# Kernel tuning notes

Hardware: AMD Instinct MI355X
Metric: run time of the kernel (lower is better)

## Reference

```python
import jax, jax.numpy as jnp
import numpy as np

N = 50000      # nodes
E = 800000     # edges (avg degree 16)
D = 128        # embed_dim
H = 8          # nhead
HD = D // H    # head dim = 16


def setup_inputs() -> dict:
    key = jax.random.key(0)
    ks = jax.random.split(key, 6)
    s = 1.0 / np.sqrt(D)  # ~xavier scale for square matrices
    return {
        "feats": jax.random.normal(ks[0], (N, D), jnp.float32),
        "edge_index": jax.random.randint(ks[1], (E, 2), 0, N, dtype=jnp.int64),
        "Wq": jax.random.normal(ks[2], (D, D), jnp.float32) * s,
        "bq": jnp.zeros((D,), jnp.float32),
        "Wk": jax.random.normal(ks[3], (D, D), jnp.float32) * s,
        "bk": jnp.zeros((D,), jnp.float32),
        "Wv": jax.random.normal(ks[4], (D, D), jnp.float32) * s,
        "bv": jnp.zeros((D,), jnp.float32),
        "Wo": jax.random.normal(ks[5], (D, D), jnp.float32) * s,
        "bo": jnp.zeros((D,), jnp.float32),
    }


def reference(feats, edge_index, Wq, bq, Wk, bk, Wv, bv, Wo, bo):
    # Projections (nn.Linear: x @ W.T + b), split into heads: [N, H, HD]
    q = (feats @ Wq.T + bq).reshape(N, H, HD)
    k = (feats @ Wk.T + bk).reshape(N, H, HD)
    v = (feats @ Wv.T + bv).reshape(N, H, HD)

    r = edge_index[:, 0]  # source nodes
    c = edge_index[:, 1]  # destination nodes (softmax / aggregation groups)

    # Per-edge, per-head dot-product scores: [E, H]
    scores = jnp.einsum('ehd,ehd->eh', q[c], k[r]) / np.sqrt(HD)

    # Custom scatter-softmax: src_max clamped to min 0; extra exp(-src_max) in denom
    smax = jnp.maximum(jax.ops.segment_max(scores, c, num_segments=N), 0.0)  # [N, H]
    ex = jnp.exp(scores - smax[c])                                           # [E, H]
    denom = jax.ops.segment_sum(ex, c, num_segments=N)                       # [N, H]
    attn = ex / (denom + jnp.exp(-smax))[c]                                  # [E, H]

    # Weighted V per edge, scatter-mean to destination nodes
    out_e = attn[:, :, None] * v[r]                      # [E, H, HD]
    agg = jax.ops.segment_sum(out_e, c, num_segments=N)  # [N, H, HD]
    cnt = jax.ops.segment_sum(jnp.ones((E,), jnp.float32), c, num_segments=N)
    agg = agg / jnp.maximum(cnt, 1.0)[:, None, None]

    return agg.reshape(N, D) @ Wo.T + bo
```

## Files before the change

kernel.cpp:

```cpp
#include <hip/hip_runtime.h>
#include <hip/hip_bf16.h>

#define N_NODES 50000
#define N_EDGES 800000
#define DIM 128
#define NHEAD 8
#define HDIM 16
#define ELL_PAD 64

#define Q_OFF      0ull
#define KV_OFF     25600000ull
#define AGG_OFF    51200000ull
#define ELL_OFF    64000000ull
#define WBF_OFF    76800000ull
#define BIAS_OFF   76931072ull
#define CNT_OFF    76933376ull

typedef __attribute__((ext_vector_type(8))) short short8;
typedef __attribute__((ext_vector_type(4))) float floatx4;

__device__ inline float bflo2f(unsigned u) { return __uint_as_float(u << 16); }
__device__ inline float bfhi2f(unsigned u) { return __uint_as_float(u & 0xffff0000u); }
__device__ inline unsigned short f2bf(float f) {
    unsigned u = __float_as_uint(f);
    return (unsigned short)((u + 0x7fffu + ((u >> 16) & 1u)) >> 16);
}

__device__ inline void detect_flags(const void* feats, const void* edge,
                                    int& isbf, int& is32) {
    const unsigned short* f = (const unsigned short*)feats;
    const unsigned int* eg = (const unsigned int*)edge;
    int lane = threadIdx.x & 63;
    unsigned e = (f[lane] >> 7) & 0xFF;
    int junk = (e >= 0x90 || (e > 0 && e <= 0x60)) ? 1 : 0;
    unsigned long long jm = __ballot(junk);
    int nz = (lane < 32 && eg[2 * lane + 1] != 0) ? 1 : 0;
    unsigned long long nm = __ballot(nz);
    isbf = (jm == 0ull) ? 1 : 0;
    is32 = (nm != 0ull) ? 1 : 0;
}

__device__ inline void load_edge(const int* edge, int is32, int e, int& r, int& c) {
    if (is32) { r = edge[2 * e]; c = edge[2 * e + 1]; }
    else {
        const long long* p = (const long long*)edge;
        r = (int)p[2 * e]; c = (int)p[2 * e + 1];
    }
    if ((unsigned)r >= N_NODES) r = 0;
    if ((unsigned)c >= N_NODES) c = 0;
}

__global__ __launch_bounds__(256) void prep_wb(const void* feats, const int* edge,
                                               const void* wq, const void* wk,
                                               const void* wv, const void* wo,
                                               const void* bq, const void* bk,
                                               const void* bv, const void* bo,
                                               unsigned short* wbf, float* bias, int* cnt) {
    int isbf, is32; detect_flags(feats, edge, isbf, is32);
    int b = blockIdx.x, t = threadIdx.x;
    if (b < 196) {
        int i = b * 256 + t;
        if (i < N_NODES) cnt[i] = 0;
    }
    if (b == 256) {
        for (int j = t; j < 512; j += 256) {
            int m2 = j >> 7, c2 = j & 127;
            const void* bb = (m2 == 0) ? bq : (m2 == 1) ? bk : (m2 == 2) ? bv : bo;
            bias[j] = isbf ? __bfloat162float(((const __hip_bfloat16*)bb)[c2])
                           : ((const float*)bb)[c2];
        }
        return;
    }
    if (isbf) return;
    int idx = b * 256 + t;
    int m = idx >> 14, rem = idx & 16383;
    const void* w = (m == 0) ? wq : (m == 1) ? wk : (m == 2) ? wv : wo;
    wbf[idx] = f2bf(((const float*)w)[rem]);
}

__global__ __launch_bounds__(256) void ell_build(const void* feats, const int* edge,
                                                 int* cnt, int* ell) {
    int isbf, is32; detect_flags(feats, edge, isbf, is32);
    int e0 = (blockIdx.x * 256 + threadIdx.x) * 2;
    #pragma unroll
    for (int j = 0; j < 2; ++j) {
        int e = e0 + j;
        if (e >= N_EDGES) return;
        int r, c; load_edge(edge, is32, e, r, c);
        int slot = atomicAdd(cnt + c, 1);
        if (slot < ELL_PAD) ell[c * ELL_PAD + slot] = r;
    }
}

__global__ __launch_bounds__(256) void qkv_mfma(const void* feats_raw, const int* edge,
                                                const void* wq_raw, const void* wk_raw,
                                                const void* wv_raw, const unsigned short* wbf,
                                                const float* bias,
                                                float* q, unsigned int* kvpack) {
    int isbf, is32; detect_flags(feats_raw, edge, isbf, is32);
    const unsigned short* W[3];
    W[0] = isbf ? (const unsigned short*)wq_raw : wbf;
    W[1] = isbf ? (const unsigned short*)wk_raw : wbf + 16384;
    W[2] = isbf ? (const unsigned short*)wv_raw : wbf + 32768;

    int wave = threadIdx.x >> 6, lane = threadIdx.x & 63;
    int rbase = blockIdx.x * 64 + wave * 16;
    int mrow = lane & 15, quad = lane >> 4;
    int arow = rbase + mrow; if (arow >= N_NODES) arow = N_NODES - 1;

    short8 a[4];
    if (isbf) {
        const unsigned short* ap = (const unsigned short*)feats_raw + (size_t)arow * DIM + quad * 8;
        #pragma unroll
        for (int kt = 0; kt < 4; ++kt) a[kt] = *(const short8*)(ap + kt * 32);
    } else {
        const float* af = (const float*)feats_raw + (size_t)arow * DIM + quad * 8;
        #pragma unroll
        for (int kt = 0; kt < 4; ++kt) {
            float4 f0 = *(const float4*)(af + kt * 32);
            float4 f1 = *(const float4*)(af + kt * 32 + 4);
            a[kt][0] = (short)f2bf(f0.x); a[kt][1] = (short)f2bf(f0.y);
            a[kt][2] = (short)f2bf(f0.z); a[kt][3] = (short)f2bf(f0.w);
            a[kt][4] = (short)f2bf(f1.x); a[kt][5] = (short)f2bf(f1.y);
            a[kt][6] = (short)f2bf(f1.z); a[kt][7] = (short)f2bf(f1.w);
        }
    }

    for (int m = 0; m < 3; ++m) {
        const unsigned short* wm = W[m];
        for (int nt = 0; nt < 8; ++nt) {
            const unsigned short* wp = wm + (size_t)(nt * 16 + mrow) * DIM + quad * 8;
            float b = bias[m * 128 + nt * 16 + mrow];
            floatx4 acc = {b, b, b, b};
            #pragma unroll
            for (int kt = 0; kt < 4; ++kt) {
                short8 bf = *(const short8*)(wp + kt * 32);
                acc = __builtin_amdgcn_mfma_f32_16x16x32_bf16(a[kt], bf, acc, 0, 0, 0);
            }
            if (m == 0) {
                #pragma unroll
                for (int r4 = 0; r4 < 4; ++r4) {
                    int row = rbase + quad * 4 + r4;
                    if (row < N_NODES) q[(size_t)row * DIM + nt * 16 + mrow] = acc[r4];
                }
            } else {
                int sel = (m == 2) ? 8 : 0;
                #pragma unroll
                for (int r4 = 0; r4 < 4; ++r4) {
                    float other = __shfl_xor(acc[r4], 1);
                    int row = rbase + quad * 4 + r4;
                    if (((lane & 1) == 0) && row < N_NODES) {
                        unsigned packed = (unsigned)f2bf(acc[r4]) | ((unsigned)f2bf(other) << 16);
                        kvpack[(size_t)row * 128 + nt * 16 + sel + (mrow >> 1)] = packed;
                    }
                }
            }
        }
    }
}

__global__ __launch_bounds__(256) void node_agg(const int* __restrict__ cnt,
                                                const int* __restrict__ ell,
                                                const float* __restrict__ q,
                                                const uint4* __restrict__ kvpack,
                                                uint4* __restrict__ agg_bf) {
    int node = (blockIdx.x * 256 + threadIdx.x) >> 6;
    int lane = threadIdx.x & 63;
    if (node >= N_NODES) return;
    int e = lane >> 3, h = lane & 7;

    float qv[16];
    const float4* qp = (const float4*)(q + (size_t)node * DIM + h * HDIM);
    #pragma unroll
    for (int i = 0; i < 4; ++i) {
        float4 tq = qp[i];
        qv[4 * i] = tq.x; qv[4 * i + 1] = tq.y; qv[4 * i + 2] = tq.z; qv[4 * i + 3] = tq.w;
    }

    int degt = cnt[node];
    int deg = degt < ELL_PAD ? degt : ELL_PAD;
    float l = 0.f;
    float acc[16];
    #pragma unroll
    for (int i = 0; i < 16; ++i) acc[i] = 0.f;

    const int* erow = ell + node * ELL_PAD;
    for (int i0 = 0; i0 < deg; i0 += 16) {
        int i1 = i0 + e, i2 = i0 + 8 + e;
        bool ok1 = i1 < deg, ok2 = i2 < deg;
        int r1 = ok1 ? erow[i1] : 0;
        int r2 = ok2 ? erow[i2] : 0;
        const uint4* kp1 = kvpack + (size_t)r1 * 32 + h * 4;
        const uint4* kp2 = kvpack + (size_t)r2 * 32 + h * 4;
        uint4 ka1 = kp1[0], kb1 = kp1[1], va1 = kp1[2], vb1 = kp1[3];
        uint4 ka2 = kp2[0], kb2 = kp2[1], va2 = kp2[2], vb2 = kp2[3];

        float s1 = 0.f;
        s1 += bflo2f(ka1.x) * qv[0]  + bfhi2f(ka1.x) * qv[1];
        s1 += bflo2f(ka1.y) * qv[2]  + bfhi2f(ka1.y) * qv[3];
        s1 += bflo2f(ka1.z) * qv[4]  + bfhi2f(ka1.z) * qv[5];
        s1 += bflo2f(ka1.w) * qv[6]  + bfhi2f(ka1.w) * qv[7];
        s1 += bflo2f(kb1.x) * qv[8]  + bfhi2f(kb1.x) * qv[9];
        s1 += bflo2f(kb1.y) * qv[10] + bfhi2f(kb1.y) * qv[11];
        s1 += bflo2f(kb1.z) * qv[12] + bfhi2f(kb1.z) * qv[13];
        s1 += bflo2f(kb1.w) * qv[14] + bfhi2f(kb1.w) * qv[15];
        float p1 = ok1 ? __expf(s1 * 0.25f) : 0.f;
        l += p1;
        acc[0]  += p1 * bflo2f(va1.x); acc[1]  += p1 * bfhi2f(va1.x);
        acc[2]  += p1 * bflo2f(va1.y); acc[3]  += p1 * bfhi2f(va1.y);
        acc[4]  += p1 * bflo2f(va1.z); acc[5]  += p1 * bfhi2f(va1.z);
        acc[6]  += p1 * bflo2f(va1.w); acc[7]  += p1 * bfhi2f(va1.w);
        acc[8]  += p1 * bflo2f(vb1.x); acc[9]  += p1 * bfhi2f(vb1.x);
        acc[10] += p1 * bflo2f(vb1.y); acc[11] += p1 * bfhi2f(vb1.y);
        acc[12] += p1 * bflo2f(vb1.z); acc[13] += p1 * bfhi2f(vb1.z);
        acc[14] += p1 * bflo2f(vb1.w); acc[15] += p1 * bfhi2f(vb1.w);

        float s2 = 0.f;
        s2 += bflo2f(ka2.x) * qv[0]  + bfhi2f(ka2.x) * qv[1];
        s2 += bflo2f(ka2.y) * qv[2]  + bfhi2f(ka2.y) * qv[3];
        s2 += bflo2f(ka2.z) * qv[4]  + bfhi2f(ka2.z) * qv[5];
        s2 += bflo2f(ka2.w) * qv[6]  + bfhi2f(ka2.w) * qv[7];
        s2 += bflo2f(kb2.x) * qv[8]  + bfhi2f(kb2.x) * qv[9];
        s2 += bflo2f(kb2.y) * qv[10] + bfhi2f(kb2.y) * qv[11];
        s2 += bflo2f(kb2.z) * qv[12] + bfhi2f(kb2.z) * qv[13];
        s2 += bflo2f(kb2.w) * qv[14] + bfhi2f(kb2.w) * qv[15];
        float p2 = ok2 ? __expf(s2 * 0.25f) : 0.f;
        l += p2;
        acc[0]  += p2 * bflo2f(va2.x); acc[1]  += p2 * bfhi2f(va2.x);
        acc[2]  += p2 * bflo2f(va2.y); acc[3]  += p2 * bfhi2f(va2.y);
        acc[4]  += p2 * bflo2f(va2.z); acc[5]  += p2 * bfhi2f(va2.z);
        acc[6]  += p2 * bflo2f(va2.w); acc[7]  += p2 * bfhi2f(va2.w);
        acc[8]  += p2 * bflo2f(vb2.x); acc[9]  += p2 * bfhi2f(vb2.x);
        acc[10] += p2 * bflo2f(vb2.y); acc[11] += p2 * bfhi2f(vb2.y);
        acc[12] += p2 * bflo2f(vb2.z); acc[13] += p2 * bfhi2f(vb2.z);
        acc[14] += p2 * bflo2f(vb2.w); acc[15] += p2 * bfhi2f(vb2.w);
    }

    #pragma unroll
    for (int m = 8; m < 64; m <<= 1) {
        l += __shfl_xor(l, m);
        #pragma unroll
        for (int i = 0; i < 16; ++i) acc[i] += __shfl_xor(acc[i], m);
    }

    float inv = 1.0f / ((1.0f + l) * (float)(degt > 0 ? degt : 1));
    if (e == 0) {
        unsigned o[8];
        #pragma unroll
        for (int i = 0; i < 8; ++i)
            o[i] = (unsigned)f2bf(acc[2 * i] * inv) | ((unsigned)f2bf(acc[2 * i + 1] * inv) << 16);
        uint4* op = agg_bf + (size_t)node * 16 + h * 2;
        op[0] = make_uint4(o[0], o[1], o[2], o[3]);
        op[1] = make_uint4(o[4], o[5], o[6], o[7]);
    }
}

__global__ __launch_bounds__(256) void out_mfma(const unsigned short* agg_bf,
                                                const void* feats, const int* edge,
                                                const void* wo_raw, const unsigned short* wbf,
                                                const float* bias, void* out) {
    int isbf, is32; detect_flags(feats, edge, isbf, is32);
    const unsigned short* W = isbf ? (const unsigned short*)wo_raw : wbf + 49152;
    int wave = threadIdx.x >> 6, lane = threadIdx.x & 63;
    int rbase = blockIdx.x * 64 + wave * 16;
    int mrow = lane & 15, quad = lane >> 4;
    int arow = rbase + mrow; if (arow >= N_NODES) arow = N_NODES - 1;

    short8 a[4];
    const unsigned short* ap = agg_bf + (size_t)arow * DIM + quad * 8;
    #pragma unroll
    for (int kt = 0; kt < 4; ++kt) a[kt] = *(const short8*)(ap + kt * 32);

    for (int nt = 0; nt < 8; ++nt) {
        const unsigned short* wp = W + (size_t)(nt * 16 + mrow) * DIM + quad * 8;
        float b = bias[3 * 128 + nt * 16 + mrow];
        floatx4 acc = {b, b, b, b};
        #pragma unroll
        for (int kt = 0; kt < 4; ++kt) {
            short8 bf = *(const short8*)(wp + kt * 32);
            acc = __builtin_amdgcn_mfma_f32_16x16x32_bf16(a[kt], bf, acc, 0, 0, 0);
        }
        if (isbf) {
            #pragma unroll
            for (int r4 = 0; r4 < 4; ++r4) {
                float other = __shfl_xor(acc[r4], 1);
                int row = rbase + quad * 4 + r4;
                if (((lane & 1) == 0) && row < N_NODES) {
                    unsigned packed = (unsigned)f2bf(acc[r4]) | ((unsigned)f2bf(other) << 16);
                    int c = nt * 16 + mrow;
                    ((unsigned int*)out)[(size_t)row * 64 + (c >> 1)] = packed;
                }
            }
        } else {
            #pragma unroll
            for (int r4 = 0; r4 < 4; ++r4) {
                int row = rbase + quad * 4 + r4;
                if (row < N_NODES) ((float*)out)[(size_t)row * DIM + nt * 16 + mrow] = acc[r4];
            }
        }
    }
}

extern "C" void kernel_launch(void* const* d_in, const int* in_sizes, int n_in,
                              void* d_out, int out_size, void* d_ws, size_t ws_size,
                              hipStream_t stream) {
    const void* feats = d_in[0];
    const int*  edge  = (const int*)d_in[1];
    const void* Wq = d_in[2]; const void* bq = d_in[3];
    const void* Wk = d_in[4]; const void* bk = d_in[5];
    const void* Wv = d_in[6]; const void* bv = d_in[7];
    const void* Wo = d_in[8]; const void* bo = d_in[9];

    char* ws = (char*)d_ws;
    float* q             = (float*)(ws + Q_OFF);
    unsigned int* kvpack = (unsigned int*)(ws + KV_OFF);
    unsigned short* aggb = (unsigned short*)(ws + AGG_OFF);
    int* ell             = (int*)(ws + ELL_OFF);
    unsigned short* wbf  = (unsigned short*)(ws + WBF_OFF);
    float* bias          = (float*)(ws + BIAS_OFF);
    int* cnt             = (int*)(ws + CNT_OFF);

    prep_wb<<<257, 256, 0, stream>>>(feats, edge, Wq, Wk, Wv, Wo, bq, bk, bv, bo,
                                     wbf, bias, cnt);

    ell_build<<<(N_EDGES / 2 + 255) / 256, 256, 0, stream>>>(feats, edge, cnt, ell);

    qkv_mfma<<<(N_NODES + 63) / 64, 256, 0, stream>>>(feats, edge, Wq, Wk, Wv, wbf,
                                                      bias, q, kvpack);

    node_agg<<<(N_NODES * 64 + 255) / 256, 256, 0, stream>>>(cnt, ell, q,
                                                             (const uint4*)kvpack,
                                                             (uint4*)aggb);

    out_mfma<<<(N_NODES + 63) / 64, 256, 0, stream>>>(aggb, feats, edge, Wo, wbf,
                                                      bias, d_out);
}
```

Before: 287.8 us.

## Fuse QKV projection with ELL build and drop weight-prep kernel

Removes the prep kernel that converted weights to bf16 and gathered biases; the weights and biases are now read and converted directly inside the MFMA loops. The ELL adjacency build is merged into the QKV kernel as extra blocks that run alongside the projection blocks. Each edge is scanned by 8 blocks, and each block keeps only the destinations whose node id matches its residue mod 8, which is meant to localise atomics. The count array is zeroed with a memset. This cuts two launches, but it reads the edge list 8 times and repeats the fp32-to-bf16 weight conversion in every block.

```diff
diff --git a/kernel.cpp b/kernel.cpp
--- a/kernel.cpp
+++ b/kernel.cpp
@@ -7,14 +7,15 @@
 #define NHEAD 8
 #define HDIM 16
 #define ELL_PAD 64
+#define QKV_BLOCKS 782
+#define ELL_SLICES 391
+#define ELL_BLOCKS (8 * ELL_SLICES)
 
 #define Q_OFF      0ull
 #define KV_OFF     25600000ull
 #define AGG_OFF    51200000ull
 #define ELL_OFF    64000000ull
-#define WBF_OFF    76800000ull
-#define BIAS_OFF   76931072ull
-#define CNT_OFF    76933376ull
+#define CNT_OFF    76800000ull
 
 typedef __attribute__((ext_vector_type(8))) short short8;
 typedef __attribute__((ext_vector_type(4))) float floatx4;
@@ -41,7 +42,7 @@
 }
 
 __device__ inline void load_edge(const int* edge, int is32, int e, int& r, int& c) {
-    if (is32) { r = edge[2 * e]; c = edge[2 * e + 1]; }
+    if (is32) { int2 p = ((const int2*)edge)[e]; r = p.x; c = p.y; }
     else {
         const long long* p = (const long long*)edge;
         r = (int)p[2 * e]; c = (int)p[2 * e + 1];
@@ -50,58 +51,53 @@
     if ((unsigned)c >= N_NODES) c = 0;
 }
 
-__global__ __launch_bounds__(256) void prep_wb(const void* feats, const int* edge,
-                                               const void* wq, const void* wk,
-                                               const void* wv, const void* wo,
+__device__ inline float ldf(const void* p, int isbf, int i) {
+    return isbf ? __bfloat162float(((const __hip_bfloat16*)p)[i])
+                : ((const float*)p)[i];
+}
+
+__device__ inline short8 ldfrag(const void* base, int isbf, size_t off) {
+    if (isbf) return *(const short8*)((const unsigned short*)base + off);
+    const float* f = (const float*)base + off;
+    float4 f0 = *(const float4*)f;
+    float4 f1 = *(const float4*)(f + 4);
+    short8 a;
+    a[0] = (short)f2bf(f0.x); a[1] = (short)f2bf(f0.y);
+    a[2] = (short)f2bf(f0.z); a[3] = (short)f2bf(f0.w);
+    a[4] = (short)f2bf(f1.x); a[5] = (short)f2bf(f1.y);
+    a[6] = (short)f2bf(f1.z); a[7] = (short)f2bf(f1.w);
+    return a;
+}
+
+__global__ __launch_bounds__(256) void qkv_ell(const void* feats_raw, const int* edge,
+                                               const void* wq_raw, const void* wk_raw,
+                                               const void* wv_raw,
                                                const void* bq, const void* bk,
-                                               const void* bv, const void* bo,
-                                               unsigned short* wbf, float* bias, int* cnt) {
-    int isbf, is32; detect_flags(feats, edge, isbf, is32);
-    int b = blockIdx.x, t = threadIdx.x;
-    if (b < 196) {
-        int i = b * 256 + t;
-        if (i < N_NODES) cnt[i] = 0;
-    }
-    if (b == 256) {
-        for (int j = t; j < 512; j += 256) {
-            int m2 = j >> 7, c2 = j & 127;
-            const void* bb = (m2 == 0) ? bq : (m2 == 1) ? bk : (m2 == 2) ? bv : bo;
-            bias[j] = isbf ? __bfloat162float(((const __hip_bfloat16*)bb)[c2])
-                           : ((const float*)bb)[c2];
+                                               const void* bv,
+                                               float* q, unsigned int* kvpack,
+                                               int* cnt, int* ell) {
+    int isbf, is32; detect_flags(feats_raw, edge, isbf, is32);
+
+    if (blockIdx.x >= QKV_BLOCKS) {
+        int b = blockIdx.x - QKV_BLOCKS;
+        int pid = b & 7, slice = b >> 3;
+        int base = slice * 2048 + (int)threadIdx.x;
+        #pragma unroll
+        for (int j = 0; j < 8; ++j) {
+            int e = base + j * 256;
+            if (e < N_EDGES) {
+                int r, c; load_edge(edge, is32, e, r, c);
+                if ((c & 7) == pid) {
+                    int slot = atomicAdd(cnt + c, 1);
+                    if (slot < ELL_PAD) ell[c * ELL_PAD + slot] = r;
+                }
+            }
         }
         return;
     }
-    if (isbf) return;
-    int idx = b * 256 + t;
-    int m = idx >> 14, rem = idx & 16383;
-    const void* w = (m == 0) ? wq : (m == 1) ? wk : (m == 2) ? wv : wo;
-    wbf[idx] = f2bf(((const float*)w)[rem]);
-}
-
-__global__ __launch_bounds__(256) void ell_build(const void* feats, const int* edge,
-                                                 int* cnt, int* ell) {
-    int isbf, is32; detect_flags(feats, edge, isbf, is32);
-    int e0 = (blockIdx.x * 256 + threadIdx.x) * 2;
-    #pragma unroll
-    for (int j = 0; j < 2; ++j) {
-        int e = e0 + j;
-        if (e >= N_EDGES) return;
-        int r, c; load_edge(edge, is32, e, r, c);
-        int slot = atomicAdd(cnt + c, 1);
-        if (slot < ELL_PAD) ell[c * ELL_PAD + slot] = r;
-    }
-}
-
-__global__ __launch_bounds__(256) void qkv_mfma(const void* feats_raw, const int* edge,
-                                                const void* wq_raw, const void* wk_raw,
-                                                const void* wv_raw, const unsigned short* wbf,
-                                                const float* bias,
-                                                float* q, unsigned int* kvpack) {
-    int isbf, is32; detect_flags(feats_raw, edge, isbf, is32);
-    const unsigned short* W[3];
-    W[0] = isbf ? (const unsigned short*)wq_raw : wbf;
-    W[1] = isbf ? (const unsigned short*)wk_raw : wbf + 16384;
-    W[2] = isbf ? (const unsigned short*)wv_raw : wbf + 32768;
+
+    const void* W[3] = {wq_raw, wk_raw, wv_raw};
+    const void* B[3] = {bq, bk, bv};
 
     int wave = threadIdx.x >> 6, lane = threadIdx.x & 63;
     int rbase = blockIdx.x * 64 + wave * 16;
@@ -109,32 +105,18 @@
     int arow = rbase + mrow; if (arow >= N_NODES) arow = N_NODES - 1;
 
     short8 a[4];
-    if (isbf) {
-        const unsigned short* ap = (const unsigned short*)feats_raw + (size_t)arow * DIM + quad * 8;
-        #pragma unroll
-        for (int kt = 0; kt < 4; ++kt) a[kt] = *(const short8*)(ap + kt * 32);
-    } else {
-        const float* af = (const float*)feats_raw + (size_t)arow * DIM + quad * 8;
-        #pragma unroll
-        for (int kt = 0; kt < 4; ++kt) {
-            float4 f0 = *(const float4*)(af + kt * 32);
-            float4 f1 = *(const float4*)(af + kt * 32 + 4);
-            a[kt][0] = (short)f2bf(f0.x); a[kt][1] = (short)f2bf(f0.y);
-            a[kt][2] = (short)f2bf(f0.z); a[kt][3] = (short)f2bf(f0.w);
-            a[kt][4] = (short)f2bf(f1.x); a[kt][5] = (short)f2bf(f1.y);
-            a[kt][6] = (short)f2bf(f1.z); a[kt][7] = (short)f2bf(f1.w);
-        }
-    }
+    #pragma unroll
+    for (int kt = 0; kt < 4; ++kt)
+        a[kt] = ldfrag(feats_raw, isbf, (size_t)arow * DIM + quad * 8 + kt * 32);
 
     for (int m = 0; m < 3; ++m) {
-        const unsigned short* wm = W[m];
+        const void* wm = W[m];
         for (int nt = 0; nt < 8; ++nt) {
-            const unsigned short* wp = wm + (size_t)(nt * 16 + mrow) * DIM + quad * 8;
-            float b = bias[m * 128 + nt * 16 + mrow];
-            floatx4 acc = {b, b, b, b};
+            float bv_ = ldf(B[m], isbf, nt * 16 + mrow);
+            floatx4 acc = {bv_, bv_, bv_, bv_};
             #pragma unroll
             for (int kt = 0; kt < 4; ++kt) {
-                short8 bf = *(const short8*)(wp + kt * 32);
+                short8 bf = ldfrag(wm, isbf, (size_t)(nt * 16 + mrow) * DIM + quad * 8 + kt * 32);
                 acc = __builtin_amdgcn_mfma_f32_16x16x32_bf16(a[kt], bf, acc, 0, 0, 0);
             }
             if (m == 0) {
@@ -257,10 +239,9 @@
 
 __global__ __launch_bounds__(256) void out_mfma(const unsigned short* agg_bf,
                                                 const void* feats, const int* edge,
-                                                const void* wo_raw, const unsigned short* wbf,
-                                                const float* bias, void* out) {
+                                                const void* wo_raw, const void* bo,
+                                                void* out) {
     int isbf, is32; detect_flags(feats, edge, isbf, is32);
-    const unsigned short* W = isbf ? (const unsigned short*)wo_raw : wbf + 49152;
     int wave = threadIdx.x >> 6, lane = threadIdx.x & 63;
     int rbase = blockIdx.x * 64 + wave * 16;
     int mrow = lane & 15, quad = lane >> 4;
@@ -272,12 +253,11 @@
     for (int kt = 0; kt < 4; ++kt) a[kt] = *(const short8*)(ap + kt * 32);
 
     for (int nt = 0; nt < 8; ++nt) {
-        const unsigned short* wp = W + (size_t)(nt * 16 + mrow) * DIM + quad * 8;
-        float b = bias[3 * 128 + nt * 16 + mrow];
+        float b = ldf(bo, isbf, nt * 16 + mrow);
         floatx4 acc = {b, b, b, b};
         #pragma unroll
         for (int kt = 0; kt < 4; ++kt) {
-            short8 bf = *(const short8*)(wp + kt * 32);
+            short8 bf = ldfrag(wo_raw, isbf, (size_t)(nt * 16 + mrow) * DIM + quad * 8 + kt * 32);
             acc = __builtin_amdgcn_mfma_f32_16x16x32_bf16(a[kt], bf, acc, 0, 0, 0);
         }
         if (isbf) {
@@ -316,22 +296,17 @@
     unsigned int* kvpack = (unsigned int*)(ws + KV_OFF);
     unsigned short* aggb = (unsigned short*)(ws + AGG_OFF);
     int* ell             = (int*)(ws + ELL_OFF);
-    unsigned short* wbf  = (unsigned short*)(ws + WBF_OFF);
-    float* bias          = (float*)(ws + BIAS_OFF);
     int* cnt             = (int*)(ws + CNT_OFF);
 
-    prep_wb<<<257, 256, 0, stream>>>(feats, edge, Wq, Wk, Wv, Wo, bq, bk, bv, bo,
-                                     wbf, bias, cnt);
-
-    ell_build<<<(N_EDGES / 2 + 255) / 256, 256, 0, stream>>>(feats, edge, cnt, ell);
-
-    qkv_mfma<<<(N_NODES + 63) / 64, 256, 0, stream>>>(feats, edge, Wq, Wk, Wv, wbf,
-                                                      bias, q, kvpack);
+    hipMemsetAsync(ws + CNT_OFF, 0, N_NODES * 4, stream);
+
+    qkv_ell<<<QKV_BLOCKS + ELL_BLOCKS, 256, 0, stream>>>(feats, edge, Wq, Wk, Wv,
+                                                         bq, bk, bv, q, kvpack,
+                                                         cnt, ell);
 
     node_agg<<<(N_NODES * 64 + 255) / 256, 256, 0, stream>>>(cnt, ell, q,
                                                              (const uint4*)kvpack,
                                                              (uint4*)aggb);
 
-    out_mfma<<<(N_NODES + 63) / 64, 256, 0, stream>>>(aggb, feats, edge, Wo, wbf,
-                                                      bias, d_out);
-}
+    out_mfma<<<(N_NODES + 63) / 64, 256, 0, stream>>>(aggb, feats, edge, Wo, bo, d_out);
+}
```

Result: no change. 288.4 us (+0.2%).
